# Optimization experiments

Hardware: AMD Instinct MI355X
Metric: run time of the kernel (lower is better)

Reference implementation:

```python
import jax, jax.numpy as jnp
import numpy as np


def setup_inputs() -> dict:
    key = jax.random.key(0)
    ks = jax.random.split(key, 6)
    B, T, dim, H = 4, 4096, 2048, 16
    s = 0.02
    x = jax.random.normal(ks[0], (B, T, dim), jnp.float32)
    w_q = jax.random.normal(ks[1], (dim, dim), jnp.float32) * s
    w_k = jax.random.normal(ks[2], (dim, dim), jnp.float32) * s
    w_v = jax.random.normal(ks[3], (dim, dim), jnp.float32) * s
    w_o = jax.random.normal(ks[4], (dim, dim), jnp.float32) * s
    w_router = jax.random.normal(ks[5], (H, dim), jnp.float32) * s
    return {"x": x, "w_q": w_q, "w_k": w_k, "w_v": w_v, "w_o": w_o,
            "w_router": w_router, "top_k": 512}


def reference(x, w_q, w_k, w_v, w_o, w_router, top_k):
    B, T, dim = x.shape
    H = w_router.shape[0]
    hd = dim // H
    K = min(top_k, T)

    # router: per-head token scores [B, H, T] -> top-k indices [B, H, K]
    router_scores = jnp.einsum('btd,hd->bht', x, w_router)
    _, idx = jax.lax.top_k(router_scores, K)

    def proj(w):
        # [B, T, dim] -> [B, H, T, hd]
        return (x @ w.T).reshape(B, T, H, hd).transpose(0, 2, 1, 3)

    q, k, v = proj(w_q), proj(w_k), proj(w_v)

    gather = lambda t: jnp.take_along_axis(t, idx[..., None], axis=2)  # [B,H,K,hd]
    q_s, k_s, v_s = gather(q), gather(k), gather(v)

    scale = hd ** -0.5
    scores = jnp.einsum('bhkd,bhld->bhkl', q_s, k_s) * scale  # [B,H,K,K]
    # causal mask on ORIGINAL positions: query pos >= key pos
    can_attend = idx[..., :, None] >= idx[..., None, :]
    scores = jnp.where(can_attend, scores, -jnp.inf)
    attn = jax.nn.softmax(scores, axis=-1)
    out_s = jnp.einsum('bhkl,bhld->bhkd', attn, v_s)  # [B,H,K,hd]

    # scatter back into zeros at selected positions (indices unique per (b,h))
    out = jnp.zeros_like(q)
    bi = jnp.arange(B)[:, None, None]
    hi = jnp.arange(H)[None, :, None]
    out = out.at[bi, hi, idx].set(out_s)

    out = out.transpose(0, 2, 1, 3).reshape(B, T, dim)
    return out @ w_o.T
```

## Files before the change

### kernel.cpp

```cpp
#include <hip/hip_runtime.h>
#include <math.h>

#define BB 4
#define TT 4096
#define DD 2048
#define HH 16
#define HDIM 128
#define KSEL 512
#define NBH (BB*HH)

using short8  = __attribute__((ext_vector_type(8))) short;
using short4v = __attribute__((ext_vector_type(4))) short;
using f32x4   = __attribute__((ext_vector_type(4))) float;

__device__ __forceinline__ short f2bf(float f) {
  unsigned u = __float_as_uint(f);
  u += 0x7fffu + ((u >> 16) & 1u);
  return (short)(u >> 16);
}
__device__ __forceinline__ float bf2f(short s) {
  return __uint_as_float(((unsigned)(unsigned short)s) << 16);
}

__device__ __forceinline__ void gload16(const short* g, short* l) {
  __builtin_amdgcn_global_load_lds(
      (const __attribute__((address_space(1))) void*)g,
      (__attribute__((address_space(3))) void*)l, 16, 0, 0);
}

__global__ __launch_bounds__(256) void k_cvt_w(const float* __restrict__ wq,
    const float* __restrict__ wk, const float* __restrict__ wv,
    const float* __restrict__ wo, short* __restrict__ dst) {
  const int wsel = blockIdx.y;
  const float* s = (wsel == 0) ? wq : (wsel == 1) ? wk : (wsel == 2) ? wv : wo;
  size_t base = (size_t)blockIdx.x * 2048 + (size_t)threadIdx.x * 8;
  float4 a = *(const float4*)(s + base);
  float4 b = *(const float4*)(s + base + 4);
  short8 o;
  o[0] = f2bf(a.x); o[1] = f2bf(a.y); o[2] = f2bf(a.z); o[3] = f2bf(a.w);
  o[4] = f2bf(b.x); o[5] = f2bf(b.y); o[6] = f2bf(b.z); o[7] = f2bf(b.w);
  *(short8*)&dst[(size_t)wsel * 4194304 + base] = o;
}

__global__ __launch_bounds__(256) void k_router2(const float* __restrict__ x,
    const float* __restrict__ wr, float* __restrict__ part,
    short* __restrict__ xb, const int writeXb) {
  __shared__ __align__(16) float Xs[128][36];
  __shared__ __align__(16) float Ws[16][36];
  const int tb = blockIdx.x, kq = blockIdx.y;
  const int tid = threadIdx.x;
  const int row0 = tb * 128;
  const int sr8 = tid >> 3, sc8 = (tid & 7) * 4;
  const int tq = tid >> 2, hq = tid & 3;
  const int kbase = kq * 256;
  float acc[2][4];
#pragma unroll
  for (int i = 0; i < 2; ++i)
#pragma unroll
    for (int j = 0; j < 4; ++j) acc[i][j] = 0.f;
  float4 xr[4], wreg;
  {
#pragma unroll
    for (int p = 0; p < 4; ++p)
      xr[p] = *(const float4*)(x + (size_t)(row0 + sr8 + p * 32) * DD + kbase + sc8);
    if (tid < 128) wreg = *(const float4*)(wr + (size_t)(tid >> 3) * DD + kbase + (tid & 7) * 4);
  }
  for (int c = 0; c < 8; ++c) {
    if (c) __syncthreads();
#pragma unroll
    for (int p = 0; p < 4; ++p) {
      *(float4*)&Xs[sr8 + p * 32][sc8] = xr[p];
      if (writeXb) {
        short4v b4;
        b4[0] = f2bf(xr[p].x); b4[1] = f2bf(xr[p].y);
        b4[2] = f2bf(xr[p].z); b4[3] = f2bf(xr[p].w);
        *(short4v*)(xb + (size_t)(row0 + sr8 + p * 32) * DD + kbase + c * 32 + sc8) = b4;
      }
    }
    if (tid < 128) *(float4*)&Ws[tid >> 3][(tid & 7) * 4] = wreg;
    __syncthreads();
    if (c < 7) {
      const int k0 = kbase + (c + 1) * 32;
#pragma unroll
      for (int p = 0; p < 4; ++p)
        xr[p] = *(const float4*)(x + (size_t)(row0 + sr8 + p * 32) * DD + k0 + sc8);
      if (tid < 128) wreg = *(const float4*)(wr + (size_t)(tid >> 3) * DD + k0 + (tid & 7) * 4);
    }
#pragma unroll
    for (int k4 = 0; k4 < 8; ++k4) {
      float4 xv0 = *(const float4*)&Xs[tq][k4 * 4];
      float4 xv1 = *(const float4*)&Xs[tq + 64][k4 * 4];
#pragma unroll
      for (int j = 0; j < 4; ++j) {
        float4 wv4 = *(const float4*)&Ws[hq + j * 4][k4 * 4];
        acc[0][j] += xv0.x * wv4.x + xv0.y * wv4.y + xv0.z * wv4.z + xv0.w * wv4.w;
        acc[1][j] += xv1.x * wv4.x + xv1.y * wv4.y + xv1.z * wv4.z + xv1.w * wv4.w;
      }
    }
  }
#pragma unroll
  for (int i = 0; i < 2; ++i) {
    int tg = row0 + tq + i * 64;
    int b = tg >> 12, t = tg & (TT - 1);
#pragma unroll
    for (int j = 0; j < 4; ++j)
      part[((size_t)kq * NBH + (b * HH + hq + j * 4)) * TT + t] = acc[i][j];
  }
}

__global__ __launch_bounds__(256) void k_router_sum(const float* __restrict__ part,
                                                    float* __restrict__ scores) {
  size_t i = ((size_t)blockIdx.x * 256 + threadIdx.x) * 4;
  const size_t S = (size_t)NBH * TT;
  float4 s = *(const float4*)(part + i);
#pragma unroll
  for (int k = 1; k < 8; ++k) {
    float4 v = *(const float4*)(part + k * S + i);
    s.x += v.x; s.y += v.y; s.z += v.z; s.w += v.w;
  }
  *(float4*)(scores + i) = s;
}

__global__ __launch_bounds__(512) void k_topk(const float* __restrict__ scores,
                                              int* __restrict__ idx,
                                              int* __restrict__ inv) {
  __shared__ unsigned hist[256];
  __shared__ unsigned ssum[257];
  __shared__ unsigned wtot[8];
  __shared__ unsigned sh_b;
  const int bh = blockIdx.x, tid = threadIdx.x;
  const int lane = tid & 63, wv = tid >> 6;
  const float* sc = scores + (size_t)bh * TT;
  unsigned key[8];
  {
    float4 v0 = *(const float4*)(sc + tid * 8);
    float4 v1 = *(const float4*)(sc + tid * 8 + 4);
    float vs[8] = {v0.x, v0.y, v0.z, v0.w, v1.x, v1.y, v1.z, v1.w};
#pragma unroll
    for (int i = 0; i < 8; ++i) {
      unsigned u = __float_as_uint(vs[i]);
      key[i] = (u & 0x80000000u) ? ~u : (u | 0x80000000u);
    }
  }
  unsigned prefix = 0, need = KSEL;
  for (int shift = 24; shift >= 0; shift -= 8) {
    if (tid < 256) hist[tid] = 0;
    __syncthreads();
#pragma unroll
    for (int i = 0; i < 8; ++i) {
      bool m = (shift == 24) || ((key[i] >> (shift + 8)) == prefix);
      if (m) atomicAdd(&hist[(key[i] >> shift) & 255], 1u);
    }
    __syncthreads();
    if (wv == 0) {
      unsigned v0 = hist[lane * 4], v1 = hist[lane * 4 + 1];
      unsigned v2 = hist[lane * 4 + 2], v3 = hist[lane * 4 + 3];
      unsigned s3 = v3, s2 = v2 + s3, s1 = v1 + s2, s0 = v0 + s1;
      unsigned t = s0;
#pragma unroll
      for (int off = 1; off < 64; off <<= 1) {
        unsigned o = __shfl_down(t, off);
        if (lane + off < 64) t += o;
      }
      unsigned above = t - s0;
      ssum[lane * 4]     = s0 + above;
      ssum[lane * 4 + 1] = s1 + above;
      ssum[lane * 4 + 2] = s2 + above;
      ssum[lane * 4 + 3] = s3 + above;
      if (lane == 0) ssum[256] = 0;
    }
    __syncthreads();
    if (tid < 256) {
      if (ssum[tid] >= need && ssum[tid + 1] < need) sh_b = (unsigned)tid;
    }
    __syncthreads();
    unsigned bstar = sh_b;
    need -= ssum[bstar + 1];
    prefix = (shift == 24) ? bstar : ((prefix << 8) | bstar);
  }
  const unsigned thr = prefix;
  unsigned cgt = 0, ceq = 0;
#pragma unroll
  for (int i = 0; i < 8; ++i) { cgt += (key[i] > thr); ceq += (key[i] == thr); }
  unsigned packed = (cgt << 16) | ceq;
  unsigned inc = packed;
#pragma unroll
  for (int off = 1; off < 64; off <<= 1) {
    unsigned o = __shfl_up(inc, off);
    if (lane >= off) inc += o;
  }
  if (lane == 63) wtot[wv] = inc;
  __syncthreads();
  unsigned wbase = 0;
#pragma unroll
  for (int w2 = 0; w2 < 8; ++w2) wbase += (w2 < wv) ? wtot[w2] : 0u;
  unsigned base = wbase + inc - packed;
  unsigned gt_before = base >> 16, eq_before = base & 0xffffu;
  int* op = idx + bh * KSEL;
  int* invrow = inv + (size_t)bh * TT;
#pragma unroll
  for (int i = 0; i < 8; ++i) {
    bool isgt = key[i] > thr, iseq = key[i] == thr;
    bool sel = isgt || (iseq && eq_before < need);
    int pos = -1;
    if (sel) {
      pos = (int)(gt_before + (eq_before < need ? eq_before : need));
      op[pos] = tid * 8 + i;
    }
    invrow[tid * 8 + i] = pos;
    gt_before += isgt; eq_before += iseq;
  }
}

template <int AB>
__global__ __launch_bounds__(256, 2) void k_qkv_mfma(
    const float* __restrict__ x, const short* __restrict__ xb,
    const short* __restrict__ wqb, const short* __restrict__ wkb,
    const short* __restrict__ wvb, const int* __restrict__ idx,
    short* __restrict__ q_s, short* __restrict__ k_s, short* __restrict__ v_t) {
  __shared__ __align__(16) short As[2][64 * 64];
  __shared__ __align__(16) short Bs[2][3][64 * 64];
  __shared__ int tIdx[64];
  const int L = blockIdx.x;
  const int xcd = L & 7;
  const int bh = xcd * 8 + (L >> 7);
  const int rt = (L >> 3) & 7;
  const int ch = (L >> 6) & 1;
  const int b = bh >> 4, h = bh & 15;
  const int tid = threadIdx.x;
  if (tid < 64) tIdx[tid] = idx[bh * KSEL + rt * 64 + tid];
  __syncthreads();
  const int lane = tid & 63, w = tid >> 6;
  const int g = lane >> 4, r15 = lane & 15;
  const int lcol8 = lane >> 3, lslot = lane & 7;
  const float* aPtr = nullptr;
  const short* aSrc0 = nullptr; const short* aSrc1 = nullptr;
  int arow = 0, rm = 0;
  if constexpr (AB) {
    int rowA0 = w * 16 + lcol8;
    aSrc0 = xb + ((size_t)b * TT + tIdx[rowA0]) * DD + ((lslot ^ lcol8) << 3);
    aSrc1 = xb + ((size_t)b * TT + tIdx[rowA0 + 8]) * DD + ((lslot ^ lcol8) << 3);
  } else {
    arow = tid >> 2;
    rm = arow & 7;
    aPtr = x + ((size_t)b * TT + tIdx[arow]) * DD + (tid & 3) * 16;
  }
  const short* wbase[3] = {wqb, wkb, wvb};
  f32x4 acc[4][3];
#pragma unroll
  for (int m = 0; m < 4; ++m)
#pragma unroll
    for (int n = 0; n < 3; ++n) acc[m][n] = (f32x4){0.f, 0.f, 0.f, 0.f};

#define STAGE(BUF, K0)                                                          \
  {                                                                             \
    if constexpr (AB) {                                                         \
      gload16(aSrc0 + (K0), &As[BUF][(w * 16) * 64]);                           \
      gload16(aSrc1 + (K0), &As[BUF][(w * 16 + 8) * 64]);                       \
    } else {                                                                    \
      float4 a0 = *(const float4*)(aPtr + (K0));                                \
      float4 a1 = *(const float4*)(aPtr + (K0) + 4);                            \
      float4 a2 = *(const float4*)(aPtr + (K0) + 8);                            \
      float4 a3 = *(const float4*)(aPtr + (K0) + 12);                           \
      short8 p0, p1;                                                            \
      p0[0] = f2bf(a0.x); p0[1] = f2bf(a0.y); p0[2] = f2bf(a0.z); p0[3] = f2bf(a0.w); \
      p0[4] = f2bf(a1.x); p0[5] = f2bf(a1.y); p0[6] = f2bf(a1.z); p0[7] = f2bf(a1.w); \
      p1[0] = f2bf(a2.x); p1[1] = f2bf(a2.y); p1[2] = f2bf(a2.z); p1[3] = f2bf(a2.w); \
      p1[4] = f2bf(a3.x); p1[5] = f2bf(a3.y); p1[6] = f2bf(a3.z); p1[7] = f2bf(a3.w); \
      int kq = tid & 3;                                                         \
      *(short8*)&As[BUF][arow * 64 + ((2 * kq) ^ rm) * 8] = p0;                 \
      *(short8*)&As[BUF][arow * 64 + ((2 * kq + 1) ^ rm) * 8] = p1;             \
    }                                                                           \
    _Pragma("unroll")                                                           \
    for (int t = 0; t < 6; ++t) {                                               \
      int gi = w * 6 + t;                                                       \
      int p = gi >> 3;                                                          \
      int c0 = (gi & 7) << 3;                                                   \
      int colg = ch * 64 + c0 + lcol8;                                          \
      const short* wsrc = wbase[p] + ((size_t)(h * HDIM + colg)) * DD + (K0)    \
                        + ((lslot ^ lcol8) << 3);                               \
      gload16(wsrc, &Bs[BUF][p][c0 * 64]);                                      \
    }                                                                           \
  }

  STAGE(0, 0);
  __syncthreads();
  int cur = 0;
  for (int k0 = 0; k0 < DD; k0 += 64) {
    if (k0 + 64 < DD) STAGE(cur ^ 1, k0 + 64);
#pragma unroll
    for (int ks = 0; ks < 2; ++ks) {
      short8 af[4], bfr[3];
#pragma unroll
      for (int m = 0; m < 4; ++m) {
        int row = m * 16 + r15;
        af[m] = *(const short8*)&As[cur][row * 64 + ((ks * 4 + g) ^ (row & 7)) * 8];
      }
#pragma unroll
      for (int n = 0; n < 3; ++n) {
        int nf = w * 3 + n;
        int coll = (nf & 3) * 16 + r15;
        bfr[n] = *(const short8*)&Bs[cur][nf >> 2][coll * 64 + ((ks * 4 + g) ^ (coll & 7)) * 8];
      }
#pragma unroll
      for (int m = 0; m < 4; ++m)
#pragma unroll
        for (int n = 0; n < 3; ++n)
          acc[m][n] = __builtin_amdgcn_mfma_f32_16x16x32_bf16(af[m], bfr[n], acc[m][n], 0, 0, 0);
    }
    __syncthreads();
    cur ^= 1;
  }
#undef STAGE

#pragma unroll
  for (int n = 0; n < 3; ++n) {
    int nf = w * 3 + n;
    int p = nf >> 2;
    int colg = ch * 64 + (nf & 3) * 16 + r15;
    if (p == 2) {
#pragma unroll
      for (int m = 0; m < 4; ++m) {
        short4v pk;
#pragma unroll
        for (int r = 0; r < 4; ++r) pk[r] = f2bf(acc[m][n][r]);
        *(short4v*)&v_t[((size_t)bh * HDIM + colg) * KSEL + rt * 64 + m * 16 + g * 4] = pk;
      }
    } else {
      short* dp = (p == 0) ? q_s : k_s;
#pragma unroll
      for (int m = 0; m < 4; ++m) {
        int row0 = rt * 64 + m * 16 + g * 4;
#pragma unroll
        for (int r = 0; r < 4; ++r)
          dp[((size_t)bh * KSEL + row0 + r) * HDIM + colg] = f2bf(acc[m][n][r]);
      }
    }
  }
}

__global__ __launch_bounds__(256) void k_attn_mfma(const short* __restrict__ q_s,
    const short* __restrict__ k_s, const short* __restrict__ v_t,
    short* __restrict__ out_s) {
  __shared__ __align__(16) short Ks[64 * 128];
  __shared__ __align__(16) short Vt[128 * 64];
  __shared__ __align__(16) short Pl[4 * 16 * 72];
  const int bh = blockIdx.x, qt = blockIdx.y;
  const int tid = threadIdx.x;
  const int w = tid >> 6, lane = tid & 63;
  const int g = lane >> 4, r15 = lane & 15;
  const size_t bhbase = (size_t)bh * KSEL * HDIM;
  const int r0 = qt * 64;
  const float scale = 0.08838834764831845f;

  short8 qf[4];
  {
    const short* qrow = q_s + bhbase + (size_t)(r0 + w * 16 + r15) * HDIM;
#pragma unroll
    for (int ks = 0; ks < 4; ++ks)
      qf[ks] = *(const short8*)(qrow + ks * 32 + g * 8);
  }
  f32x4 o[8];
#pragma unroll
  for (int n = 0; n < 8; ++n) o[n] = (f32x4){0.f, 0.f, 0.f, 0.f};
  float mrow[4] = {-INFINITY, -INFINITY, -INFINITY, -INFINITY};
  float lrow[4] = {0.f, 0.f, 0.f, 0.f};

  short* myP = &Pl[w * 16 * 72];
  const int kl16 = lane >> 4, ks16 = lane & 15;
  const int vl8 = lane >> 3, vs8 = lane & 7;

  for (int kt = 0; kt <= qt; ++kt) {
    int l0 = kt * 64;
    __syncthreads();
    {
#pragma unroll
      for (int t = 0; t < 4; ++t) {
        int gi = w * 4 + t;
        int kr0 = gi * 4;
        int key = kr0 + kl16;
        const short* ksrc = k_s + bhbase + (size_t)(l0 + key) * HDIM + ((ks16 ^ (key & 7)) << 3);
        gload16(ksrc, &Ks[kr0 * 128]);
        int d0 = gi * 8;
        int d = d0 + vl8;
        const short* vsrc = v_t + ((size_t)bh * HDIM + d) * KSEL + l0 + ((vs8 ^ (d & 7)) << 3);
        gload16(vsrc, &Vt[d0 * 64]);
      }
    }
    __syncthreads();

    f32x4 s[4];
#pragma unroll
    for (int n = 0; n < 4; ++n) s[n] = (f32x4){0.f, 0.f, 0.f, 0.f};
#pragma unroll
    for (int ks = 0; ks < 4; ++ks) {
#pragma unroll
      for (int n = 0; n < 4; ++n) {
        int row = n * 16 + r15;
        short8 kf = *(const short8*)&Ks[row * 128 + ((ks * 4 + g) ^ (r15 & 7)) * 8];
        s[n] = __builtin_amdgcn_mfma_f32_16x16x32_bf16(qf[ks], kf, s[n], 0, 0, 0);
      }
    }

    const bool diag = (kt == qt);
    float sv[4][4];
#pragma unroll
    for (int n = 0; n < 4; ++n) {
      int key = kt * 64 + n * 16 + r15;
#pragma unroll
      for (int r = 0; r < 4; ++r) {
        float xv = s[n][r] * scale;
        int qrow = r0 + w * 16 + g * 4 + r;
        sv[n][r] = (diag && key > qrow) ? -INFINITY : xv;
      }
    }
    float corr[4];
#pragma unroll
    for (int r = 0; r < 4; ++r) {
      float tm = fmaxf(fmaxf(sv[0][r], sv[1][r]), fmaxf(sv[2][r], sv[3][r]));
#pragma unroll
      for (int off = 8; off; off >>= 1) tm = fmaxf(tm, __shfl_xor(tm, off));
      float newm = fmaxf(mrow[r], tm);
      corr[r] = __expf(mrow[r] - newm);
      mrow[r] = newm;
      float ps = 0.f;
#pragma unroll
      for (int n = 0; n < 4; ++n) {
        float pv = __expf(sv[n][r] - newm);
        sv[n][r] = pv;
        ps += pv;
      }
#pragma unroll
      for (int off = 8; off; off >>= 1) ps += __shfl_xor(ps, off);
      lrow[r] = lrow[r] * corr[r] + ps;
    }
    f32x4 corrv = {corr[0], corr[1], corr[2], corr[3]};
#pragma unroll
    for (int n = 0; n < 4; ++n)
#pragma unroll
      for (int r = 0; r < 4; ++r)
        myP[(g * 4 + r) * 72 + n * 16 + r15] = f2bf(sv[n][r]);
#pragma unroll
    for (int n = 0; n < 8; ++n) o[n] *= corrv;

    short8 pf[2];
#pragma unroll
    for (int ks = 0; ks < 2; ++ks)
      pf[ks] = *(const short8*)&myP[r15 * 72 + ks * 32 + g * 8];
#pragma unroll
    for (int ks = 0; ks < 2; ++ks)
#pragma unroll
      for (int n2 = 0; n2 < 8; ++n2) {
        int row = n2 * 16 + r15;
        short8 vf = *(const short8*)&Vt[row * 64 + ((ks * 4 + g) ^ (r15 & 7)) * 8];
        o[n2] = __builtin_amdgcn_mfma_f32_16x16x32_bf16(pf[ks], vf, o[n2], 0, 0, 0);
      }
  }

  float inv[4];
#pragma unroll
  for (int r = 0; r < 4; ++r) inv[r] = 1.f / lrow[r];
#pragma unroll
  for (int n2 = 0; n2 < 8; ++n2) {
#pragma unroll
    for (int r = 0; r < 4; ++r) {
      int qrow = r0 + w * 16 + g * 4 + r;
      out_s[bhbase + (size_t)qrow * HDIM + n2 * 16 + r15] = f2bf(o[n2][r] * inv[r]);
    }
  }
}

__global__ __launch_bounds__(256) void k_oproj_p1(
    const short* __restrict__ out_s_b, const short* __restrict__ wob,
    short* __restrict__ P) {
  __shared__ __align__(16) short As[128 * 64];
  __shared__ __align__(16) short Bs[128 * 64];
  const int h = blockIdx.x, rt = blockIdx.y, ct = blockIdx.z;
  const int tid = threadIdx.x;
  const int lane = tid & 63, wid = tid >> 6;
  const int wr = wid >> 1, wc = wid & 1;
  const int l8 = lane >> 3, s8 = lane & 7;
  f32x4 acc[4][4];
#pragma unroll
  for (int m = 0; m < 4; ++m)
#pragma unroll
    for (int n = 0; n < 4; ++n) acc[m][n] = (f32x4){0.f, 0.f, 0.f, 0.f};
  const int r15 = lane & 15, g = lane >> 4;
#pragma unroll
  for (int k0 = 0; k0 < HDIM; k0 += 64) {
    __syncthreads();
    {
#pragma unroll
      for (int t = 0; t < 4; ++t) {
        int gi = wid * 4 + t;
        int r0 = gi * 8;
        int row = r0 + l8;
        const short* asrc = out_s_b + ((size_t)h * KSEL + rt * 128 + row) * HDIM + k0
                          + ((s8 ^ (row & 7)) << 3);
        gload16(asrc, &As[r0 * 64]);
        const short* bsrc = wob + ((size_t)(ct * 128 + row)) * DD + h * HDIM + k0
                          + ((s8 ^ (row & 7)) << 3);
        gload16(bsrc, &Bs[r0 * 64]);
      }
    }
    __syncthreads();
#pragma unroll
    for (int ks = 0; ks < 2; ++ks) {
      short8 af[4], bfr[4];
#pragma unroll
      for (int m = 0; m < 4; ++m) {
        int row = wr * 64 + m * 16 + r15;
        int chunk = (ks * 4 + g) ^ (row & 7);
        af[m] = *(const short8*)&As[row * 64 + chunk * 8];
      }
#pragma unroll
      for (int n = 0; n < 4; ++n) {
        int col = wc * 64 + n * 16 + r15;
        int chunk = (ks * 4 + g) ^ (col & 7);
        bfr[n] = *(const short8*)&Bs[col * 64 + chunk * 8];
      }
#pragma unroll
      for (int m = 0; m < 4; ++m)
#pragma unroll
        for (int n = 0; n < 4; ++n)
          acc[m][n] = __builtin_amdgcn_mfma_f32_16x16x32_bf16(af[m], bfr[n], acc[m][n], 0, 0, 0);
    }
  }
#pragma unroll
  for (int m = 0; m < 4; ++m) {
#pragma unroll
    for (int r = 0; r < 4; ++r) {
      int row = rt * 128 + wr * 64 + m * 16 + g * 4 + r;
#pragma unroll
      for (int n = 0; n < 4; ++n) {
        int col = ct * 128 + wc * 64 + n * 16 + r15;
        P[((size_t)h * KSEL + row) * DD + col] = f2bf(acc[m][n][r]);
      }
    }
  }
}

__global__ __launch_bounds__(256) void k_oproj_p2(const short* __restrict__ P,
    const int* __restrict__ inv_b, float* __restrict__ out_b) {
  const int t = blockIdx.x, tid = threadIdx.x;
  const int c0 = tid * 8;
  float acc[8] = {0.f, 0.f, 0.f, 0.f, 0.f, 0.f, 0.f, 0.f};
#pragma unroll
  for (int h = 0; h < HH; ++h) {
    int k = inv_b[h * TT + t];
    if (k >= 0) {
      short8 pv = *(const short8*)&P[((size_t)h * KSEL + k) * DD + c0];
#pragma unroll
      for (int e = 0; e < 8; ++e) acc[e] += bf2f(pv[e]);
    }
  }
  float4 o0 = {acc[0], acc[1], acc[2], acc[3]};
  float4 o1 = {acc[4], acc[5], acc[6], acc[7]};
  *(float4*)&out_b[(size_t)t * DD + c0] = o0;
  *(float4*)&out_b[(size_t)t * DD + c0 + 4] = o1;
}

extern "C" void kernel_launch(void* const* d_in, const int* in_sizes, int n_in,
                              void* d_out, int out_size, void* d_ws, size_t ws_size,
                              hipStream_t stream) {
  (void)in_sizes; (void)n_in; (void)out_size;
  const float* x  = (const float*)d_in[0];
  const float* wq = (const float*)d_in[1];
  const float* wk = (const float*)d_in[2];
  const float* wv = (const float*)d_in[3];
  const float* wo = (const float*)d_in[4];
  const float* wr = (const float*)d_in[5];
  float* out = (float*)d_out;

  char* ws = (char*)d_ws;
  float* scores = (float*)ws;
  int*   idx    = (int*)(ws + 1048576);
  short* wqb    = (short*)(ws + 1179648);
  short* wkb    = wqb + 4194304;
  short* wvb    = wkb + 4194304;
  short* wob    = wvb + 4194304;
  short* out_s  = wob + 4194304;
  int*   inv    = (int*)((char*)out_s + 8388608);
  short* P      = (short*)((char*)inv + 1048576);
  short* q_s    = P;
  short* k_s    = P + 4194304;
  short* v_t    = P + 8388608;
  float* part   = (float*)P;
  const size_t NEED_XB = 144834560ULL;
  const int big = (ws_size >= NEED_XB) ? 1 : 0;
  short* xb = big ? (short*)(ws + 77725696) : (short*)ws;

  k_cvt_w<<<dim3(2048, 4), 256, 0, stream>>>(wq, wk, wv, wo, wqb);
  k_router2<<<dim3(128, 8), 256, 0, stream>>>(x, wr, part, xb, big);
  k_router_sum<<<256, 256, 0, stream>>>(part, scores);
  k_topk<<<NBH, 512, 0, stream>>>(scores, idx, inv);
  if (big)
    k_qkv_mfma<1><<<1024, 256, 0, stream>>>(x, xb, wqb, wkb, wvb, idx, q_s, k_s, v_t);
  else
    k_qkv_mfma<0><<<1024, 256, 0, stream>>>(x, xb, wqb, wkb, wvb, idx, q_s, k_s, v_t);
  k_attn_mfma<<<dim3(NBH, KSEL / 64), 256, 0, stream>>>(q_s, k_s, v_t, out_s);
  for (int b = 0; b < BB; ++b) {
    k_oproj_p1<<<dim3(HH, KSEL / 128, DD / 128), 256, 0, stream>>>(
        out_s + (size_t)b * HH * KSEL * HDIM, wob, P);
    k_oproj_p2<<<TT, 256, 0, stream>>>(
        P, inv + (size_t)b * HH * TT, out + (size_t)b * TT * DD);
  }
}
```

Measured before the change: 298.9 us.

## Load QKV weight fragments directly from global memory and widen N-tile per block

The QKV projection kernel stops staging weight tiles through shared memory. Each wave now reads its B fragments straight from global memory into registers. Each block covers all 128 head columns across Q/K/V (6 N-fragments per wave), so the grid is halved to 512 blocks and the activation tile is loaded once per block instead of twice. This removes LDS traffic and the shared-memory footprint for weights, but adds register pressure (24 accumulators) and puts uncoalesced, unpipelined global loads on the MFMA critical path.

```diff
diff --git a/kernel.cpp b/kernel.cpp
--- a/kernel.cpp
+++ b/kernel.cpp
@@ -219,13 +219,11 @@
     const short* __restrict__ wvb, const int* __restrict__ idx,
     short* __restrict__ q_s, short* __restrict__ k_s, short* __restrict__ v_t) {
   __shared__ __align__(16) short As[2][64 * 64];
-  __shared__ __align__(16) short Bs[2][3][64 * 64];
   __shared__ int tIdx[64];
   const int L = blockIdx.x;
   const int xcd = L & 7;
-  const int bh = xcd * 8 + (L >> 7);
+  const int bh = xcd * 8 + (L >> 6);
   const int rt = (L >> 3) & 7;
-  const int ch = (L >> 6) & 1;
   const int b = bh >> 4, h = bh & 15;
   const int tid = threadIdx.x;
   if (tid < 64) tIdx[tid] = idx[bh * KSEL + rt * 64 + tid];
@@ -245,14 +243,22 @@
     rm = arow & 7;
     aPtr = x + ((size_t)b * TT + tIdx[arow]) * DD + (tid & 3) * 16;
   }
-  const short* wbase[3] = {wqb, wkb, wvb};
-  f32x4 acc[4][3];
+  const short* bptr[6];
+#pragma unroll
+  for (int n = 0; n < 6; ++n) {
+    int nf = w * 6 + n;
+    int p = nf >> 3;
+    const short* wb = (p == 0) ? wqb : (p == 1) ? wkb : wvb;
+    int col = (nf & 7) * 16 + r15;
+    bptr[n] = wb + ((size_t)(h * HDIM + col)) * DD + g * 8;
+  }
+  f32x4 acc[4][6];
 #pragma unroll
   for (int m = 0; m < 4; ++m)
 #pragma unroll
-    for (int n = 0; n < 3; ++n) acc[m][n] = (f32x4){0.f, 0.f, 0.f, 0.f};
-
-#define STAGE(BUF, K0)                                                          \
+    for (int n = 0; n < 6; ++n) acc[m][n] = (f32x4){0.f, 0.f, 0.f, 0.f};
+
+#define STAGE_A(BUF, K0)                                                        \
   {                                                                             \
     if constexpr (AB) {                                                         \
       gload16(aSrc0 + (K0), &As[BUF][(w * 16) * 64]);                           \
@@ -271,60 +277,47 @@
       *(short8*)&As[BUF][arow * 64 + ((2 * kq) ^ rm) * 8] = p0;                 \
       *(short8*)&As[BUF][arow * 64 + ((2 * kq + 1) ^ rm) * 8] = p1;             \
     }                                                                           \
-    _Pragma("unroll")                                                           \
-    for (int t = 0; t < 6; ++t) {                                               \
-      int gi = w * 6 + t;                                                       \
-      int p = gi >> 3;                                                          \
-      int c0 = (gi & 7) << 3;                                                   \
-      int colg = ch * 64 + c0 + lcol8;                                          \
-      const short* wsrc = wbase[p] + ((size_t)(h * HDIM + colg)) * DD + (K0)    \
-                        + ((lslot ^ lcol8) << 3);                               \
-      gload16(wsrc, &Bs[BUF][p][c0 * 64]);                                      \
-    }                                                                           \
-  }
-
-  STAGE(0, 0);
+  }
+
+  STAGE_A(0, 0);
   __syncthreads();
   int cur = 0;
   for (int k0 = 0; k0 < DD; k0 += 64) {
-    if (k0 + 64 < DD) STAGE(cur ^ 1, k0 + 64);
+    if (k0 + 64 < DD) STAGE_A(cur ^ 1, k0 + 64);
 #pragma unroll
     for (int ks = 0; ks < 2; ++ks) {
-      short8 af[4], bfr[3];
+      short8 af[4], bfr[6];
+#pragma unroll
+      for (int n = 0; n < 6; ++n)
+        bfr[n] = *(const short8*)(bptr[n] + k0 + ks * 32);
 #pragma unroll
       for (int m = 0; m < 4; ++m) {
         int row = m * 16 + r15;
         af[m] = *(const short8*)&As[cur][row * 64 + ((ks * 4 + g) ^ (row & 7)) * 8];
       }
 #pragma unroll
-      for (int n = 0; n < 3; ++n) {
-        int nf = w * 3 + n;
-        int coll = (nf & 3) * 16 + r15;
-        bfr[n] = *(const short8*)&Bs[cur][nf >> 2][coll * 64 + ((ks * 4 + g) ^ (coll & 7)) * 8];
-      }
-#pragma unroll
       for (int m = 0; m < 4; ++m)
 #pragma unroll
-        for (int n = 0; n < 3; ++n)
+        for (int n = 0; n < 6; ++n)
           acc[m][n] = __builtin_amdgcn_mfma_f32_16x16x32_bf16(af[m], bfr[n], acc[m][n], 0, 0, 0);
     }
     __syncthreads();
     cur ^= 1;
   }
-#undef STAGE
-
-#pragma unroll
-  for (int n = 0; n < 3; ++n) {
-    int nf = w * 3 + n;
-    int p = nf >> 2;
-    int colg = ch * 64 + (nf & 3) * 16 + r15;
+#undef STAGE_A
+
+#pragma unroll
+  for (int n = 0; n < 6; ++n) {
+    int nf = w * 6 + n;
+    int p = nf >> 3;
+    int col = (nf & 7) * 16 + r15;
     if (p == 2) {
 #pragma unroll
       for (int m = 0; m < 4; ++m) {
         short4v pk;
 #pragma unroll
         for (int r = 0; r < 4; ++r) pk[r] = f2bf(acc[m][n][r]);
-        *(short4v*)&v_t[((size_t)bh * HDIM + colg) * KSEL + rt * 64 + m * 16 + g * 4] = pk;
+        *(short4v*)&v_t[((size_t)bh * HDIM + col) * KSEL + rt * 64 + m * 16 + g * 4] = pk;
       }
     } else {
       short* dp = (p == 0) ? q_s : k_s;
@@ -333,7 +326,7 @@
         int row0 = rt * 64 + m * 16 + g * 4;
 #pragma unroll
         for (int r = 0; r < 4; ++r)
-          dp[((size_t)bh * KSEL + row0 + r) * HDIM + colg] = f2bf(acc[m][n][r]);
+          dp[((size_t)bh * KSEL + row0 + r) * HDIM + col] = f2bf(acc[m][n][r]);
       }
     }
   }
@@ -595,9 +588,9 @@
   k_router_sum<<<256, 256, 0, stream>>>(part, scores);
   k_topk<<<NBH, 512, 0, stream>>>(scores, idx, inv);
   if (big)
-    k_qkv_mfma<1><<<1024, 256, 0, stream>>>(x, xb, wqb, wkb, wvb, idx, q_s, k_s, v_t);
+    k_qkv_mfma<1><<<512, 256, 0, stream>>>(x, xb, wqb, wkb, wvb, idx, q_s, k_s, v_t);
   else
-    k_qkv_mfma<0><<<1024, 256, 0, stream>>>(x, xb, wqb, wkb, wvb, idx, q_s, k_s, v_t);
+    k_qkv_mfma<0><<<512, 256, 0, stream>>>(x, xb, wqb, wkb, wvb, idx, q_s, k_s, v_t);
   k_attn_mfma<<<dim3(NBH, KSEL / 64), 256, 0, stream>>>(q_s, k_s, v_t, out_s);
   for (int b = 0; b < BB; ++b) {
     k_oproj_p1<<<dim3(HH, KSEL / 128, DD / 128), 256, 0, stream>>>(
```

New measurement: 324.8 us. 8.6% more time.
